# Performance work log

Measured on AMD Instinct MI355X. Metric: run time of the kernel, lower is better.

## Reference

```python
import jax, jax.numpy as jnp
import numpy as np

# Grid constants from point_cloud_range and PILLAR_SIZE (KITTI PointPillars defaults)
PX, PY, PZ = 0.16, 0.16, 4.0
X0, Y0, Z0 = 0.0, -39.68, -3.0
NX, NY, NZ = 432, 496, 1
X_OFF = PX / 2 + X0
Y_OFF = PY / 2 + Y0
Z_OFF = PZ / 2 + Z0
B = 8          # batch size
P = 96000      # total pillars across batch
M = 32         # max points per pillar
CIN = 10       # 4 base + 3 cluster + 3 center
COUT = 64      # FILTERS[-1]
BN_EPS = 1e-3


def setup_inputs() -> dict:
    key = jax.random.key(0)
    k1, k2, k3, k4, k5, k6 = jax.random.split(key, 6)
    pillars = jax.random.normal(k1, (P, M, 4), dtype=jnp.float32)
    b = jax.random.randint(k2, (P,), 0, B, dtype=jnp.int32)
    z = jnp.zeros((P,), dtype=jnp.int32)  # nz == 1
    y = jax.random.randint(k3, (P,), 0, NY, dtype=jnp.int32)
    x = jax.random.randint(k4, (P,), 0, NX, dtype=jnp.int32)
    coords = jnp.stack([b, z, y, x], axis=1)  # (P, 4) as [batch, z, y, x]
    num_points = jax.random.randint(k5, (P,), 1, M + 1, dtype=jnp.int32)
    W = jax.random.normal(k6, (CIN, COUT), dtype=jnp.float32) * 0.05
    gamma = jnp.ones((COUT,), dtype=jnp.float32)
    beta = jnp.zeros((COUT,), dtype=jnp.float32)
    return {"pillars": pillars, "coords": coords, "num_points": num_points,
            "W": W, "gamma": gamma, "beta": beta}


def _pfe_forward(pillars, W, gamma, beta, coords, num_points):
    # --- feature augmentation ---
    abs_xyz = pillars[:, :, :3]                                   # (P, M, 3)
    n = num_points.astype(pillars.dtype)[:, None, None]
    mean_xyz = jnp.sum(abs_xyz, axis=1, keepdims=True) / n        # (P, 1, 3)
    xyz_to_cluster = abs_xyz - mean_xyz                           # (P, M, 3)
    cz = coords[:, 1].astype(pillars.dtype)
    cy = coords[:, 2].astype(pillars.dtype)
    cx = coords[:, 3].astype(pillars.dtype)
    centers = jnp.stack([cx * PX + X_OFF, cy * PY + Y_OFF, cz * PZ + Z_OFF], axis=-1)
    xyz_to_center = abs_xyz - centers[:, None, :]                 # (P, M, 3)
    feats = jnp.concatenate([pillars, xyz_to_cluster, xyz_to_center], axis=-1)  # (P, M, 10)

    # --- PFNLayer: linear (no bias) + BatchNorm1d (train-mode batch stats) + ReLU + max over points ---
    h = jnp.einsum("pmi,io->pmo", feats, W)                       # (P, M, COUT)
    mu = jnp.mean(h, axis=(0, 1))
    var = jnp.var(h, axis=(0, 1))                                 # biased, like torch BN
    h = (h - mu) * jax.lax.rsqrt(var + BN_EPS) * gamma + beta
    h = jax.nn.relu(h)
    pv = jnp.max(h, axis=1)                                       # (P, COUT)

    # --- scatter pillar features to dense BEV grid ---
    cell = coords[:, 1] + coords[:, 2] * NX + coords[:, 3]        # z + y*nx + x
    flat = coords[:, 0] * (NZ * NY * NX) + cell                   # (P,)
    bev = jnp.zeros((B * NZ * NY * NX, COUT), dtype=pv.dtype).at[flat].set(pv)
    bev = bev.reshape(B, NZ * NY * NX, COUT).transpose(0, 2, 1)   # (B, C, nz*ny*nx)
    return bev.reshape(B, COUT * NZ, NY, NX)


def reference(pillars, coords, num_points, W, gamma, beta):
    return _pfe_forward(pillars, W, gamma, beta, coords, num_points)
```

## Files before the change

### kernel.cpp

```cpp
#include <hip/hip_runtime.h>

#define NPILLARS 96000
#define MPTS 32
#define NCHAN 64
#define NXC 432
#define NYC 496
#define NB 8
#define NCELLS (NXC*NYC)
#define NBLK 1024
#define PXc 0.16f
#define PYc 0.16f
#define PZc 4.0f
#define XOFF (0.08f)
#define YOFF (0.08f - 39.68f)
#define ZOFF (2.0f - 3.0f)
#define BN_EPS 1e-3f

typedef __attribute__((ext_vector_type(8))) short short8;
typedef __attribute__((ext_vector_type(16))) float float16;

__device__ __forceinline__ short f2bf(float x) {
    union { float f; unsigned u; } v; v.f = x;
    unsigned r = v.u + 0x7FFFu + ((v.u >> 16) & 1u);
    return (short)(r >> 16);
}

#define PAIRS(Q) \
 Q(0,0,0) Q(1,0,1) Q(2,0,2) Q(3,0,3) Q(4,0,4) Q(5,0,5) Q(6,0,6) Q(7,0,7) Q(8,0,8) Q(9,0,9) \
 Q(10,1,1) Q(11,1,2) Q(12,1,3) Q(13,1,4) Q(14,1,5) Q(15,1,6) Q(16,1,7) Q(17,1,8) Q(18,1,9) \
 Q(19,2,2) Q(20,2,3) Q(21,2,4) Q(22,2,5) Q(23,2,6) Q(24,2,7) Q(25,2,8) Q(26,2,9) \
 Q(27,3,3) Q(28,3,4) Q(29,3,5) Q(30,3,6) Q(31,3,7) Q(32,3,8) Q(33,3,9) \
 Q(34,4,4) Q(35,4,5) Q(36,4,6) Q(37,4,7) Q(38,4,8) Q(39,4,9) \
 Q(40,5,5) Q(41,5,6) Q(42,5,7) Q(43,5,8) Q(44,5,9) \
 Q(45,6,6) Q(46,6,7) Q(47,6,8) Q(48,6,9) \
 Q(49,7,7) Q(50,7,8) Q(51,7,9) \
 Q(52,8,8) Q(53,8,9) \
 Q(54,9,9)

__global__ __launch_bounds__(256, 3)
void k_fused(const float4* __restrict__ pillars,
             const int4* __restrict__ coords,
             const int* __restrict__ num_points,
             const float* __restrict__ W,
             float* __restrict__ pvmax,
             float* __restrict__ pvmin,
             float* __restrict__ partial,
             int* __restrict__ winner) {
    const int tid  = threadIdx.x;
    const int lane = tid & 63;
    const int sub  = lane & 31;
    const int half = lane >> 5;
    const int wv   = tid >> 6;
    const int wid    = (blockIdx.x * blockDim.x + tid) >> 6;
    const int nwaves = (gridDim.x * blockDim.x) >> 6;

    short8 bf0, bf1;
#pragma unroll
    for (int r = 0; r < 8; r++) {
        const int k = half * 8 + r;
        bf0[r] = (k < 10) ? f2bf(W[k * NCHAN + sub])      : (short)0;
        bf1[r] = (k < 10) ? f2bf(W[k * NCHAN + 32 + sub]) : (short)0;
    }

    float s0=0.f,s1=0.f,s2=0.f,s3=0.f,s4=0.f,s5=0.f,s6=0.f,s7=0.f,s8=0.f,s9=0.f;
#define QDECL(idx,i,j) float q_##i##_##j = 0.f;
    PAIRS(QDECL)
#undef QDECL

    for (int p = wid; p < NPILLARS; p += nwaves) {
        float4 pt = pillars[p * MPTS + sub];
        float sx = pt.x, sy = pt.y, sz = pt.z;
#pragma unroll
        for (int m = 16; m >= 1; m >>= 1) {
            sx += __shfl_xor(sx, m);
            sy += __shfl_xor(sy, m);
            sz += __shfl_xor(sz, m);
        }
        const float n = (float)num_points[p];
        const float mx = sx / n, my = sy / n, mz = sz / n;
        const int4  cd = coords[p];
        const float ctx = (float)cd.w * PXc + XOFF;
        const float cty = (float)cd.z * PYc + YOFF;
        const float ctz = (float)cd.y * PZc + ZOFF;
        const float f0=pt.x, f1=pt.y, f2=pt.z, f3=pt.w;
        const float f4=pt.x-mx,  f5=pt.y-my,  f6=pt.z-mz;
        const float f7=pt.x-ctx, f8=pt.y-cty, f9=pt.z-ctz;
        s0+=f0; s1+=f1; s2+=f2; s3+=f3; s4+=f4;
        s5+=f5; s6+=f6; s7+=f7; s8+=f8; s9+=f9;
#define QACC(idx,i,j) q_##i##_##j = fmaf(f##i, f##j, q_##i##_##j);
        PAIRS(QACC)
#undef QACC
        const short b0 = f2bf(f0), b1 = f2bf(f1), b2 = f2bf(f2), b3 = f2bf(f3),
                    b4 = f2bf(f4), b5 = f2bf(f5), b6 = f2bf(f6), b7 = f2bf(f7),
                    b8 = f2bf(f8), b9 = f2bf(f9);
        short8 a;
        a[0] = half ? b8 : b0;
        a[1] = half ? b9 : b1;
        a[2] = half ? (short)0 : b2;
        a[3] = half ? (short)0 : b3;
        a[4] = half ? (short)0 : b4;
        a[5] = half ? (short)0 : b5;
        a[6] = half ? (short)0 : b6;
        a[7] = half ? (short)0 : b7;
        float16 acc0 = {};
        float16 acc1 = {};
        acc0 = __builtin_amdgcn_mfma_f32_32x32x16_bf16(a, bf0, acc0, 0, 0, 0);
        acc1 = __builtin_amdgcn_mfma_f32_32x32x16_bf16(a, bf1, acc1, 0, 0, 0);
        float mx0 = -3.4e38f, mx1 = -3.4e38f, mn0 = 3.4e38f, mn1 = 3.4e38f;
#pragma unroll
        for (int r = 0; r < 16; r++) {
            mx0 = fmaxf(mx0, acc0[r]);  mn0 = fminf(mn0, acc0[r]);
            mx1 = fmaxf(mx1, acc1[r]);  mn1 = fminf(mn1, acc1[r]);
        }
        mx0 = fmaxf(mx0, __shfl_xor(mx0, 32));  mn0 = fminf(mn0, __shfl_xor(mn0, 32));
        mx1 = fmaxf(mx1, __shfl_xor(mx1, 32));  mn1 = fminf(mn1, __shfl_xor(mn1, 32));
        pvmax[p * NCHAN + lane] = half ? mx1 : mx0;
        pvmin[p * NCHAN + lane] = half ? mn1 : mn0;
        if (lane == 0) {
            const int cell = cd.y + cd.z * NXC + cd.w;
            atomicMax(&winner[cd.x * NCELLS + cell], p);
        }
    }

    __shared__ float lds_part[4][65];
#define RED6(v) { v += __shfl_xor(v,32); v += __shfl_xor(v,16); v += __shfl_xor(v,8); \
                  v += __shfl_xor(v,4);  v += __shfl_xor(v,2);  v += __shfl_xor(v,1); }
    RED6(s0) RED6(s1) RED6(s2) RED6(s3) RED6(s4)
    RED6(s5) RED6(s6) RED6(s7) RED6(s8) RED6(s9)
#define QRED(idx,i,j) RED6(q_##i##_##j)
    PAIRS(QRED)
#undef QRED
#undef RED6
    if (lane == 0) {
        float* dst = &lds_part[wv][0];
        dst[0]=s0; dst[1]=s1; dst[2]=s2; dst[3]=s3; dst[4]=s4;
        dst[5]=s5; dst[6]=s6; dst[7]=s7; dst[8]=s8; dst[9]=s9;
#define QST(idx,i,j) dst[10+idx] = q_##i##_##j;
        PAIRS(QST)
#undef QST
    }
    __syncthreads();
    if (tid < 65) {
        const float acc = lds_part[0][tid] + lds_part[1][tid]
                        + lds_part[2][tid] + lds_part[3][tid];
        partial[tid * NBLK + blockIdx.x] = acc;
    }
}

__global__ void k_finalize(const float* __restrict__ partial,
                           const float* __restrict__ W,
                           const float* __restrict__ gamma,
                           const float* __restrict__ beta,
                           float* __restrict__ ss) {
    __shared__ float mom[65];
    const int tid = threadIdx.x;
    if (tid < 65) mom[tid] = 0.f;
    __syncthreads();
    for (int task = tid; task < 65 * 4; task += 256) {
        const int i = task >> 2, ch = task & 3;
        const float4* p4 = (const float4*)(partial + (size_t)i * NBLK) + ch * (NBLK/16);
        float a0=0.f, a1=0.f, a2=0.f, a3=0.f;
#pragma unroll 8
        for (int b = 0; b < NBLK/16; b++) {
            float4 v = p4[b];
            a0 += v.x; a1 += v.y; a2 += v.z; a3 += v.w;
        }
        atomicAdd(&mom[i], (a0 + a1) + (a2 + a3));
    }
    __syncthreads();
    const int c = tid;
    if (c >= 64) return;
    const double invN = 1.0 / (2.0 * (double)NPILLARS * (double)MPTS);
    double wv[10];
#pragma unroll
    for (int i = 0; i < 10; i++) wv[i] = (double)W[i * NCHAN + c];
    double mu = 0.0;
#pragma unroll
    for (int i = 0; i < 10; i++) mu += (double)mom[i] * wv[i];
    mu *= invN;
    double e2 = 0.0;
#define QFOLD(idx,i,j) { double t = (double)mom[10+idx] * wv[i] * wv[j]; \
                         e2 += (i == j) ? t : 2.0 * t; }
    PAIRS(QFOLD)
#undef QFOLD
    e2 *= invN;
    const double var = e2 - mu * mu;
    const float scale = (float)((double)gamma[c] / sqrt(var + (double)BN_EPS));
    const float shift = beta[c] - (float)mu * scale;
    ss[c] = scale;
    ss[64 + c] = shift;
}

__global__ void k_expand(const int* __restrict__ winner,
                         const float* __restrict__ pvmax,
                         const float* __restrict__ pvmin,
                         const float* __restrict__ ss,
                         float* __restrict__ out) {
    __shared__ float s_sc[64], s_sh[64];
    const int t = threadIdx.x;
    if (t < 64) s_sc[t] = ss[t];
    else if (t < 128) s_sh[t - 64] = ss[t];
    __syncthreads();
    const int idx = blockIdx.x * blockDim.x + t;
    const int total4 = NB * NCELLS / 4;
    if (idx >= total4) return;
    const int b    = (idx << 2) / NCELLS;
    const int cell = (idx << 2) - b * NCELLS;
    const int4 w = ((const int4*)winner)[idx];
    float* obase = out + (size_t)b * NCHAN * NCELLS + cell;
#pragma unroll 4
    for (int c = 0; c < NCHAN; c++) {
        const float sc = s_sc[c], sh = s_sh[c];
        const float* buf = (sc >= 0.f) ? pvmax : pvmin;
        float4 v;
        v.x = (w.x >= 0) ? fmaxf(0.f, fmaf(buf[w.x * NCHAN + c], sc, sh)) : 0.f;
        v.y = (w.y >= 0) ? fmaxf(0.f, fmaf(buf[w.y * NCHAN + c], sc, sh)) : 0.f;
        v.z = (w.z >= 0) ? fmaxf(0.f, fmaf(buf[w.z * NCHAN + c], sc, sh)) : 0.f;
        v.w = (w.w >= 0) ? fmaxf(0.f, fmaf(buf[w.w * NCHAN + c], sc, sh)) : 0.f;
        *reinterpret_cast<float4*>(obase + (size_t)c * NCELLS) = v;
    }
}

extern "C" void kernel_launch(void* const* d_in, const int* in_sizes, int n_in,
                              void* d_out, int out_size, void* d_ws, size_t ws_size,
                              hipStream_t stream) {
    const float4* pillars    = (const float4*)d_in[0];
    const int4*   coords     = (const int4*)d_in[1];
    const int*    num_points = (const int*)d_in[2];
    const float*  W          = (const float*)d_in[3];
    const float*  gamma      = (const float*)d_in[4];
    const float*  beta       = (const float*)d_in[5];
    float* out = (float*)d_out;

    char* ws = (char*)d_ws;
    const size_t PV_BYTES = (size_t)NPILLARS * NCHAN * sizeof(float);
    float* ss      = (float*)ws;
    int*   winner  = (int*)(ws + 4096);
    float* pvmax   = (float*)(ws + 4096 + (size_t)NB*NCELLS*4);
    float* pvmin   = (float*)((char*)pvmax + PV_BYTES);
    float* partial = (float*)((char*)pvmin + PV_BYTES);

    (void)hipMemsetAsync(winner, 0xFF, (size_t)NB * NCELLS * sizeof(int), stream);

    k_fused   <<<NBLK, 256, 0, stream>>>(pillars, coords, num_points, W,
                                         pvmax, pvmin, partial, winner);
    k_finalize<<<1, 256, 0, stream>>>(partial, W, gamma, beta, ss);
    k_expand  <<<(NB * NCELLS / 4 + 255) / 256, 256, 0, stream>>>(winner, pvmax, pvmin, ss, out);
}
```

Measured before the change: 585.7 us.

## Fold BN finalize into expand kernel and vectorize pillar-feature gathers

Removes the single-block finalize kernel. Block partial moments are now reduced with global atomicAdd into a small buffer, and every expand block recomputes the BN scale and shift from those moments in float instead of double. The expand kernel now gathers four channels per float4 load per pillar and reads pvmin only for channel groups with a negative scale. Winner indices are shifted by one so a single memset zeroes both the moments and the winner grid. This saves one launch and the scalar per-channel gathers, at the cost of redundant per-block BN math, atomic contention, and some loss of precision in the variance.

```diff
diff --git a/kernel.cpp b/kernel.cpp
--- a/kernel.cpp
+++ b/kernel.cpp
@@ -18,6 +18,7 @@
 
 typedef __attribute__((ext_vector_type(8))) short short8;
 typedef __attribute__((ext_vector_type(16))) float float16;
+typedef __attribute__((ext_vector_type(4))) float natf4;
 
 __device__ __forceinline__ short f2bf(float x) {
     union { float f; unsigned u; } v; v.f = x;
@@ -44,7 +45,7 @@
              const float* __restrict__ W,
              float* __restrict__ pvmax,
              float* __restrict__ pvmin,
-             float* __restrict__ partial,
+             float* __restrict__ mom,
              int* __restrict__ winner) {
     const int tid  = threadIdx.x;
     const int lane = tid & 63;
@@ -118,7 +119,7 @@
         pvmin[p * NCHAN + lane] = half ? mn1 : mn0;
         if (lane == 0) {
             const int cell = cd.y + cd.z * NXC + cd.w;
-            atomicMax(&winner[cd.x * NCELLS + cell], p);
+            atomicMax(&winner[cd.x * NCELLS + cell], p + 1);
         }
     }
 
@@ -143,81 +144,94 @@
     if (tid < 65) {
         const float acc = lds_part[0][tid] + lds_part[1][tid]
                         + lds_part[2][tid] + lds_part[3][tid];
-        partial[tid * NBLK + blockIdx.x] = acc;
-    }
-}
-
-__global__ void k_finalize(const float* __restrict__ partial,
-                           const float* __restrict__ W,
-                           const float* __restrict__ gamma,
-                           const float* __restrict__ beta,
-                           float* __restrict__ ss) {
-    __shared__ float mom[65];
-    const int tid = threadIdx.x;
-    if (tid < 65) mom[tid] = 0.f;
-    __syncthreads();
-    for (int task = tid; task < 65 * 4; task += 256) {
-        const int i = task >> 2, ch = task & 3;
-        const float4* p4 = (const float4*)(partial + (size_t)i * NBLK) + ch * (NBLK/16);
-        float a0=0.f, a1=0.f, a2=0.f, a3=0.f;
-#pragma unroll 8
-        for (int b = 0; b < NBLK/16; b++) {
-            float4 v = p4[b];
-            a0 += v.x; a1 += v.y; a2 += v.z; a3 += v.w;
-        }
-        atomicAdd(&mom[i], (a0 + a1) + (a2 + a3));
-    }
-    __syncthreads();
-    const int c = tid;
-    if (c >= 64) return;
-    const double invN = 1.0 / (2.0 * (double)NPILLARS * (double)MPTS);
-    double wv[10];
-#pragma unroll
-    for (int i = 0; i < 10; i++) wv[i] = (double)W[i * NCHAN + c];
-    double mu = 0.0;
-#pragma unroll
-    for (int i = 0; i < 10; i++) mu += (double)mom[i] * wv[i];
-    mu *= invN;
-    double e2 = 0.0;
-#define QFOLD(idx,i,j) { double t = (double)mom[10+idx] * wv[i] * wv[j]; \
-                         e2 += (i == j) ? t : 2.0 * t; }
-    PAIRS(QFOLD)
-#undef QFOLD
-    e2 *= invN;
-    const double var = e2 - mu * mu;
-    const float scale = (float)((double)gamma[c] / sqrt(var + (double)BN_EPS));
-    const float shift = beta[c] - (float)mu * scale;
-    ss[c] = scale;
-    ss[64 + c] = shift;
+        atomicAdd(&mom[tid], acc);
+    }
 }
 
 __global__ void k_expand(const int* __restrict__ winner,
                          const float* __restrict__ pvmax,
                          const float* __restrict__ pvmin,
-                         const float* __restrict__ ss,
+                         const float* __restrict__ mom,
+                         const float* __restrict__ W,
+                         const float* __restrict__ gamma,
+                         const float* __restrict__ beta,
                          float* __restrict__ out) {
     __shared__ float s_sc[64], s_sh[64];
+    __shared__ int s_neg[16];
     const int t = threadIdx.x;
-    if (t < 64) s_sc[t] = ss[t];
-    else if (t < 128) s_sh[t - 64] = ss[t];
+    if (t < 64) {
+        const float invN = 1.0f / (2.0f * (float)NPILLARS * (float)MPTS);
+        float wv0=W[0*NCHAN+t], wv1=W[1*NCHAN+t], wv2=W[2*NCHAN+t], wv3=W[3*NCHAN+t],
+              wv4=W[4*NCHAN+t], wv5=W[5*NCHAN+t], wv6=W[6*NCHAN+t], wv7=W[7*NCHAN+t],
+              wv8=W[8*NCHAN+t], wv9=W[9*NCHAN+t];
+        float mu = mom[0]*wv0 + mom[1]*wv1 + mom[2]*wv2 + mom[3]*wv3 + mom[4]*wv4
+                 + mom[5]*wv5 + mom[6]*wv6 + mom[7]*wv7 + mom[8]*wv8 + mom[9]*wv9;
+        mu *= invN;
+        float e2 = 0.f;
+#define QFOLD(idx,i,j) { float tt = mom[10+idx] * wv##i * wv##j; \
+                         e2 += (i == j) ? tt : 2.0f * tt; }
+        PAIRS(QFOLD)
+#undef QFOLD
+        e2 *= invN;
+        const float var = e2 - mu * mu;
+        const float scale = gamma[t] * rsqrtf(var + BN_EPS);
+        const float shift = beta[t] - mu * scale;
+        s_sc[t] = scale;
+        s_sh[t] = shift;
+    }
     __syncthreads();
+    if (t < 16) {
+        s_neg[t] = (s_sc[4*t] < 0.f) | (s_sc[4*t+1] < 0.f)
+                 | (s_sc[4*t+2] < 0.f) | (s_sc[4*t+3] < 0.f);
+    }
+    __syncthreads();
+
     const int idx = blockIdx.x * blockDim.x + t;
     const int total4 = NB * NCELLS / 4;
     if (idx >= total4) return;
     const int b    = (idx << 2) / NCELLS;
     const int cell = (idx << 2) - b * NCELLS;
     const int4 w = ((const int4*)winner)[idx];
+    const float mk0 = (w.x > 0) ? 1.f : 0.f;
+    const float mk1 = (w.y > 0) ? 1.f : 0.f;
+    const float mk2 = (w.z > 0) ? 1.f : 0.f;
+    const float mk3 = (w.w > 0) ? 1.f : 0.f;
+    const size_t r0 = (size_t)((w.x > 0) ? w.x - 1 : 0) * NCHAN;
+    const size_t r1 = (size_t)((w.y > 0) ? w.y - 1 : 0) * NCHAN;
+    const size_t r2 = (size_t)((w.z > 0) ? w.z - 1 : 0) * NCHAN;
+    const size_t r3 = (size_t)((w.w > 0) ? w.w - 1 : 0) * NCHAN;
     float* obase = out + (size_t)b * NCHAN * NCELLS + cell;
-#pragma unroll 4
-    for (int c = 0; c < NCHAN; c++) {
-        const float sc = s_sc[c], sh = s_sh[c];
-        const float* buf = (sc >= 0.f) ? pvmax : pvmin;
-        float4 v;
-        v.x = (w.x >= 0) ? fmaxf(0.f, fmaf(buf[w.x * NCHAN + c], sc, sh)) : 0.f;
-        v.y = (w.y >= 0) ? fmaxf(0.f, fmaf(buf[w.y * NCHAN + c], sc, sh)) : 0.f;
-        v.z = (w.z >= 0) ? fmaxf(0.f, fmaf(buf[w.z * NCHAN + c], sc, sh)) : 0.f;
-        v.w = (w.w >= 0) ? fmaxf(0.f, fmaf(buf[w.w * NCHAN + c], sc, sh)) : 0.f;
-        *reinterpret_cast<float4*>(obase + (size_t)c * NCELLS) = v;
+#pragma unroll 2
+    for (int g = 0; g < 16; g++) {
+        natf4 a0 = *(const natf4*)(pvmax + r0 + 4*g);
+        natf4 a1 = *(const natf4*)(pvmax + r1 + 4*g);
+        natf4 a2 = *(const natf4*)(pvmax + r2 + 4*g);
+        natf4 a3 = *(const natf4*)(pvmax + r3 + 4*g);
+        if (s_neg[g]) {
+            natf4 n0 = *(const natf4*)(pvmin + r0 + 4*g);
+            natf4 n1 = *(const natf4*)(pvmin + r1 + 4*g);
+            natf4 n2 = *(const natf4*)(pvmin + r2 + 4*g);
+            natf4 n3 = *(const natf4*)(pvmin + r3 + 4*g);
+#pragma unroll
+            for (int j = 0; j < 4; j++) {
+                const bool pos = s_sc[4*g + j] >= 0.f;
+                a0[j] = pos ? a0[j] : n0[j];
+                a1[j] = pos ? a1[j] : n1[j];
+                a2[j] = pos ? a2[j] : n2[j];
+                a3[j] = pos ? a3[j] : n3[j];
+            }
+        }
+#pragma unroll
+        for (int j = 0; j < 4; j++) {
+            const int c = 4*g + j;
+            const float sc = s_sc[c], sh = s_sh[c];
+            natf4 v;
+            v.x = mk0 * fmaxf(0.f, fmaf(a0[j], sc, sh));
+            v.y = mk1 * fmaxf(0.f, fmaf(a1[j], sc, sh));
+            v.z = mk2 * fmaxf(0.f, fmaf(a2[j], sc, sh));
+            v.w = mk3 * fmaxf(0.f, fmaf(a3[j], sc, sh));
+            *reinterpret_cast<natf4*>(obase + (size_t)c * NCELLS) = v;
+        }
     }
 }
 
@@ -233,17 +247,17 @@
     float* out = (float*)d_out;
 
     char* ws = (char*)d_ws;
-    const size_t PV_BYTES = (size_t)NPILLARS * NCHAN * sizeof(float);
-    float* ss      = (float*)ws;
-    int*   winner  = (int*)(ws + 4096);
-    float* pvmax   = (float*)(ws + 4096 + (size_t)NB*NCELLS*4);
-    float* pvmin   = (float*)((char*)pvmax + PV_BYTES);
-    float* partial = (float*)((char*)pvmin + PV_BYTES);
-
-    (void)hipMemsetAsync(winner, 0xFF, (size_t)NB * NCELLS * sizeof(int), stream);
-
-    k_fused   <<<NBLK, 256, 0, stream>>>(pillars, coords, num_points, W,
-                                         pvmax, pvmin, partial, winner);
-    k_finalize<<<1, 256, 0, stream>>>(partial, W, gamma, beta, ss);
-    k_expand  <<<(NB * NCELLS / 4 + 255) / 256, 256, 0, stream>>>(winner, pvmax, pvmin, ss, out);
-}
+    const size_t WIN_BYTES = (size_t)NB * NCELLS * sizeof(int);
+    const size_t PV_BYTES  = (size_t)NPILLARS * NCHAN * sizeof(float);
+    float* mom    = (float*)ws;
+    int*   winner = (int*)(ws + 512);
+    float* pvmax  = (float*)(ws + 512 + WIN_BYTES);
+    float* pvmin  = (float*)((char*)pvmax + PV_BYTES);
+
+    (void)hipMemsetAsync(ws, 0, 512 + WIN_BYTES, stream);
+
+    k_fused <<<NBLK, 256, 0, stream>>>(pillars, coords, num_points, W,
+                                       pvmax, pvmin, mom, winner);
+    k_expand<<<(NB * NCELLS / 4) / 256, 256, 0, stream>>>(winner, pvmax, pvmin,
+                                                          mom, W, gamma, beta, out);
+}
```

Result: faster. 560.9 us (-4.2%).
